# Kernel optimization log

Measured on AMD Instinct MI355X. Metric: run time of the kernel, lower is better.

Reference implementation:

```python
import jax, jax.numpy as jnp
import numpy as np

# Representation config (from init_kwargs): rep1 = rep2 = degrees [0, 1], mult = 32
N = 50000          # nodes
E = 800000         # edges (avg degree 16)
M = 32             # channel multiplicity (rep2.mult)
L_IN = [0, 1]
L_OUT = [0, 1]
D_IN = sum(2 * l + 1 for l in L_IN)    # 4; rep1_cdims = [0, 1, 4]
D_OUT = sum(2 * l + 1 for l in L_OUT)  # 4
OUT_DIMS = np.array([2 * l + 1 for l in L_OUT])  # [1, 3]


def setup_inputs() -> dict:
    key = jax.random.key(0)
    k1, k2, k3, k4 = jax.random.split(key, 4)
    basis = jax.random.normal(k1, (E, D_OUT, D_IN), dtype=jnp.float32)
    edge_weights = jax.random.normal(k2, (E, len(L_OUT), M), dtype=jnp.float32)
    node_features = jax.random.normal(k3, (N, D_IN, M), dtype=jnp.float32)
    U = jax.random.randint(k4, (E,), 0, N)  # edge source node indices
    return {"basis": basis, "edge_weights": edge_weights,
            "node_features": node_features, "U": U}


def reference(basis, edge_weights, node_features, U):
    # matmulStepOne: gather source-node features per edge, contract with the
    # per-edge equivariant basis (block-structured over rep1 degree slices;
    # equivalent to one dense [D_OUT, D_IN] matmul per edge).
    x = node_features[U]                          # [E, D_IN, M] (irregular gather)
    tmp = jnp.einsum('eoi,eim->eom', basis, x)    # [E, D_OUT, M]
    # matmulStepTwo: degree-wise weighted combine — each output degree block
    # (of size 2l+1) is scaled by its per-edge, per-channel radial weight.
    w = jnp.repeat(edge_weights, OUT_DIMS, axis=1, total_repeat_length=D_OUT)  # [E, D_OUT, M]
    return tmp * w
```

## Files before the change

### kernel.cpp

```cpp
#include <hip/hip_runtime.h>


typedef float f4 __attribute__((ext_vector_type(4)));

__global__ __launch_bounds__(256) void equiv_mm_kernel(
    const float* __restrict__ basis,
    const float* __restrict__ ew,
    const float* __restrict__ nf,
    const int*   __restrict__ U,
    float*       __restrict__ out,
    int E)
{
    int gid = blockIdx.x * blockDim.x + threadIdx.x;
    int e = gid >> 3;
    if (e >= E) return;
    int m0 = (gid & 7) << 2;

    int u = U[e];

    const f4* xp = (const f4*)(nf + (size_t)u * 128 + m0);
    f4 x0 = xp[0];
    f4 x1 = xp[8];
    f4 x2 = xp[16];
    f4 x3 = xp[24];

    const f4* bp = (const f4*)(basis + (size_t)e * 16);
    f4 b0 = __builtin_nontemporal_load(bp + 0);
    f4 b1 = __builtin_nontemporal_load(bp + 1);
    f4 b2 = __builtin_nontemporal_load(bp + 2);
    f4 b3 = __builtin_nontemporal_load(bp + 3);

    const f4* wp = (const f4*)(ew + (size_t)e * 64 + m0);
    f4 w0 = __builtin_nontemporal_load(wp + 0);
    f4 w1 = __builtin_nontemporal_load(wp + 8);

    f4* op = (f4*)(out + (size_t)e * 128 + m0);
    __builtin_nontemporal_store((b0.x * x0 + b0.y * x1 + b0.z * x2 + b0.w * x3) * w0, op + 0);
    __builtin_nontemporal_store((b1.x * x0 + b1.y * x1 + b1.z * x2 + b1.w * x3) * w1, op + 8);
    __builtin_nontemporal_store((b2.x * x0 + b2.y * x1 + b2.z * x2 + b2.w * x3) * w1, op + 16);
    __builtin_nontemporal_store((b3.x * x0 + b3.y * x1 + b3.z * x2 + b3.w * x3) * w1, op + 24);
}

extern "C" void kernel_launch(void* const* d_in, const int* in_sizes, int n_in,
                              void* d_out, int out_size, void* d_ws, size_t ws_size,
                              hipStream_t stream) {
    const float* basis = (const float*)d_in[0];
    const float* ew    = (const float*)d_in[1];
    const float* nf    = (const float*)d_in[2];
    const int*   U     = (const int*)d_in[3];
    float* out = (float*)d_out;

    int E = in_sizes[0] / 16;
    long long total = (long long)E * 8;
    int block = 256;
    int grid = (int)((total + block - 1) / block);

    equiv_mm_kernel<<<grid, block, 0, stream>>>(basis, ew, nf, U, out, E);
}
```

Measured before the change: 153.7 us.

## Partition edges into node-range passes to keep gathered features cache-resident

Splits the work into passes by source-node range (4096 nodes per pass). Each block scans its 256 edges and processes only those whose source node falls in the current pass, so the gathered node features for one pass stay within a cache-sized window. The cost is that every pass re-reads the whole U array, roughly 13 passes, and many waves do little useful work because of divergence. Output writes become scattered across passes instead of streaming in order.

```diff
diff --git a/kernel.cpp b/kernel.cpp
--- a/kernel.cpp
+++ b/kernel.cpp
@@ -3,42 +3,57 @@
 
 typedef float f4 __attribute__((ext_vector_type(4)));
 
-__global__ __launch_bounds__(256) void equiv_mm_kernel(
+#define NSHIFT 12
+#define EDGES_PER_BLOCK 256
+
+__global__ __launch_bounds__(256) void equiv_mm_pass_kernel(
     const float* __restrict__ basis,
     const float* __restrict__ ew,
     const float* __restrict__ nf,
     const int*   __restrict__ U,
     float*       __restrict__ out,
-    int E)
+    int E, int blocksPerPass)
 {
-    int gid = blockIdx.x * blockDim.x + threadIdx.x;
-    int e = gid >> 3;
-    if (e >= E) return;
-    int m0 = (gid & 7) << 2;
+    const int pass  = blockIdx.x / blocksPerPass;
+    const int blk   = blockIdx.x % blocksPerPass;
+    const int group = threadIdx.x >> 3;
+    const int m0    = (threadIdx.x & 7) << 2;
+    const int ebase = blk * EDGES_PER_BLOCK;
 
-    int u = U[e];
+    #pragma unroll 1
+    for (int it = 0; it < 8; ++it) {
+        int e = ebase + it * 32 + group;
+        int u = 0;
+        bool active = false;
+        if (e < E) {
+            u = U[e];
+            active = ((u >> NSHIFT) == pass);
+        }
+        if (__ballot(active) == 0ull) continue;
+        if (!active) continue;
 
-    const f4* xp = (const f4*)(nf + (size_t)u * 128 + m0);
-    f4 x0 = xp[0];
-    f4 x1 = xp[8];
-    f4 x2 = xp[16];
-    f4 x3 = xp[24];
+        const f4* xp = (const f4*)(nf + (size_t)u * 128 + m0);
+        f4 x0 = xp[0];
+        f4 x1 = xp[8];
+        f4 x2 = xp[16];
+        f4 x3 = xp[24];
 
-    const f4* bp = (const f4*)(basis + (size_t)e * 16);
-    f4 b0 = __builtin_nontemporal_load(bp + 0);
-    f4 b1 = __builtin_nontemporal_load(bp + 1);
-    f4 b2 = __builtin_nontemporal_load(bp + 2);
-    f4 b3 = __builtin_nontemporal_load(bp + 3);
+        const f4* bp = (const f4*)(basis + (size_t)e * 16);
+        f4 b0 = __builtin_nontemporal_load(bp + 0);
+        f4 b1 = __builtin_nontemporal_load(bp + 1);
+        f4 b2 = __builtin_nontemporal_load(bp + 2);
+        f4 b3 = __builtin_nontemporal_load(bp + 3);
 
-    const f4* wp = (const f4*)(ew + (size_t)e * 64 + m0);
-    f4 w0 = __builtin_nontemporal_load(wp + 0);
-    f4 w1 = __builtin_nontemporal_load(wp + 8);
+        const f4* wp = (const f4*)(ew + (size_t)e * 64 + m0);
+        f4 w0 = __builtin_nontemporal_load(wp + 0);
+        f4 w1 = __builtin_nontemporal_load(wp + 8);
 
-    f4* op = (f4*)(out + (size_t)e * 128 + m0);
-    __builtin_nontemporal_store((b0.x * x0 + b0.y * x1 + b0.z * x2 + b0.w * x3) * w0, op + 0);
-    __builtin_nontemporal_store((b1.x * x0 + b1.y * x1 + b1.z * x2 + b1.w * x3) * w1, op + 8);
-    __builtin_nontemporal_store((b2.x * x0 + b2.y * x1 + b2.z * x2 + b2.w * x3) * w1, op + 16);
-    __builtin_nontemporal_store((b3.x * x0 + b3.y * x1 + b3.z * x2 + b3.w * x3) * w1, op + 24);
+        f4* op = (f4*)(out + (size_t)e * 128 + m0);
+        __builtin_nontemporal_store((b0.x * x0 + b0.y * x1 + b0.z * x2 + b0.w * x3) * w0, op + 0);
+        __builtin_nontemporal_store((b1.x * x0 + b1.y * x1 + b1.z * x2 + b1.w * x3) * w1, op + 8);
+        __builtin_nontemporal_store((b2.x * x0 + b2.y * x1 + b2.z * x2 + b2.w * x3) * w1, op + 16);
+        __builtin_nontemporal_store((b3.x * x0 + b3.y * x1 + b3.z * x2 + b3.w * x3) * w1, op + 24);
+    }
 }
 
 extern "C" void kernel_launch(void* const* d_in, const int* in_sizes, int n_in,
@@ -51,9 +66,11 @@
     float* out = (float*)d_out;
 
     int E = in_sizes[0] / 16;
-    long long total = (long long)E * 8;
-    int block = 256;
-    int grid = (int)((total + block - 1) / block);
+    int N = in_sizes[2] / 128;
+    int npass = ((N - 1) >> NSHIFT) + 1;
+    int blocksPerPass = (E + EDGES_PER_BLOCK - 1) / EDGES_PER_BLOCK;
+    int grid = blocksPerPass * npass;
 
-    equiv_mm_kernel<<<grid, block, 0, stream>>>(basis, ew, nf, U, out, E);
+    equiv_mm_pass_kernel<<<grid, 256, 0, stream>>>(basis, ew, nf, U, out,
+                                                   E, blocksPerPass);
 }
```

Result: slower. 347.7 us (+126.3%).

## Bucket edges by source node block and stage node features in LDS

Applied to the files above, without the earlier changes.

Adds histogram, scan and scatter kernels that group edges by 64-node blocks of their source node. A bucketed kernel then loads each node slice into shared memory and processes that bucket's edges from LDS. The aim is to remove the irregular global gather of node features. In exchange it adds extra launches, contended atomics and a permuted access pattern over the large per-edge arrays.

```diff
diff --git a/kernel.cpp b/kernel.cpp
--- a/kernel.cpp
+++ b/kernel.cpp
@@ -3,42 +3,123 @@
 
 typedef float f4 __attribute__((ext_vector_type(4)));
 
-__global__ __launch_bounds__(256) void equiv_mm_kernel(
+#define BSHIFT 6
+#define BBLK 512
+
+
+__global__ void hist_kernel(const int* __restrict__ U, int* __restrict__ hist, int E) {
+    int stride = gridDim.x * blockDim.x;
+    for (int e = blockIdx.x * blockDim.x + threadIdx.x; e < E; e += stride)
+        atomicAdd(&hist[U[e] >> BSHIFT], 1);
+}
+
+__global__ void scan_kernel(int* __restrict__ hist ,
+                            int* __restrict__ cursor , int NB, int E) {
+    __shared__ int a[1024], b[1024];
+    int t = threadIdx.x;
+    a[t] = (t < NB) ? hist[t] : 0;
+    __syncthreads();
+    int* src = a; int* dst = b;
+    for (int off = 1; off < 1024; off <<= 1) {
+        int x = src[t];
+        if (t >= off) x += src[t - off];
+        dst[t] = x;
+        __syncthreads();
+        int* tmp = src; src = dst; dst = tmp;
+    }
+    if (t < NB) {
+        int excl = (t == 0) ? 0 : src[t - 1];
+        hist[t] = excl;
+        cursor[t] = excl;
+    }
+    if (t == 0) hist[NB] = E;
+}
+
+__global__ void scatter_kernel(const int* __restrict__ U, int* __restrict__ cursor,
+                               int* __restrict__ perm, int E) {
+    int stride = gridDim.x * blockDim.x;
+    for (int e = blockIdx.x * blockDim.x + threadIdx.x; e < E; e += stride) {
+        int u = U[e];
+        int pos = atomicAdd(&cursor[u >> BSHIFT], 1);
+        perm[pos] = ((u & ((1 << BSHIFT) - 1)) << 24) | e;
+    }
+}
+
+
+__global__ __launch_bounds__(BBLK) void equiv_mm_bucket_kernel(
     const float* __restrict__ basis,
     const float* __restrict__ ew,
     const float* __restrict__ nf,
-    const int*   __restrict__ U,
+    const int*   __restrict__ base,
+    const int*   __restrict__ perm,
     float*       __restrict__ out,
-    int E)
+    int N, int NB)
+{
+    __shared__ f4 slice[(1 << BSHIFT) * 32];
+    const f4* nf4 = (const f4*)nf;
+
+    for (int nb = blockIdx.x; nb < NB; nb += gridDim.x) {
+        int node0 = nb << BSHIFT;
+        int nNodes = min(1 << BSHIFT, N - node0);
+        int cnt4 = nNodes * 32;
+        __syncthreads();
+        for (int i = threadIdx.x; i < cnt4; i += BBLK)
+            slice[i] = __builtin_nontemporal_load(&nf4[(size_t)node0 * 32 + i]);
+        __syncthreads();
+
+        int start = base[nb], end = base[nb + 1];
+        int lanes = (end - start) << 3;
+        for (int k = threadIdx.x; k < lanes; k += BBLK) {
+            int slot = start + (k >> 3);
+            int m0 = (k & 7) << 2;
+            int pk = __builtin_nontemporal_load(&perm[slot]);
+            int e  = pk & 0xFFFFFF;
+            int ul = pk >> 24;
+
+            const f4* xp = slice + ul * 32 + (m0 >> 2);
+            f4 x0 = xp[0], x1 = xp[8], x2 = xp[16], x3 = xp[24];
+
+            const f4* bp = (const f4*)(basis + (size_t)e * 16);
+            f4 b0 = __builtin_nontemporal_load(bp + 0);
+            f4 b1 = __builtin_nontemporal_load(bp + 1);
+            f4 b2 = __builtin_nontemporal_load(bp + 2);
+            f4 b3 = __builtin_nontemporal_load(bp + 3);
+
+            const f4* wp = (const f4*)(ew + (size_t)e * 64 + m0);
+            f4 w0 = __builtin_nontemporal_load(wp + 0);
+            f4 w1 = __builtin_nontemporal_load(wp + 8);
+
+            f4* op = (f4*)(out + (size_t)e * 128 + m0);
+            __builtin_nontemporal_store((b0.x*x0 + b0.y*x1 + b0.z*x2 + b0.w*x3) * w0, op + 0);
+            __builtin_nontemporal_store((b1.x*x0 + b1.y*x1 + b1.z*x2 + b1.w*x3) * w1, op + 8);
+            __builtin_nontemporal_store((b2.x*x0 + b2.y*x1 + b2.z*x2 + b2.w*x3) * w1, op + 16);
+            __builtin_nontemporal_store((b3.x*x0 + b3.y*x1 + b3.z*x2 + b3.w*x3) * w1, op + 24);
+        }
+    }
+}
+
+
+__global__ __launch_bounds__(256) void equiv_mm_simple_kernel(
+    const float* __restrict__ basis, const float* __restrict__ ew,
+    const float* __restrict__ nf, const int* __restrict__ U,
+    float* __restrict__ out, int E)
 {
     int gid = blockIdx.x * blockDim.x + threadIdx.x;
     int e = gid >> 3;
     if (e >= E) return;
     int m0 = (gid & 7) << 2;
-
     int u = U[e];
-
     const f4* xp = (const f4*)(nf + (size_t)u * 128 + m0);
-    f4 x0 = xp[0];
-    f4 x1 = xp[8];
-    f4 x2 = xp[16];
-    f4 x3 = xp[24];
-
+    f4 x0 = xp[0], x1 = xp[8], x2 = xp[16], x3 = xp[24];
     const f4* bp = (const f4*)(basis + (size_t)e * 16);
-    f4 b0 = __builtin_nontemporal_load(bp + 0);
-    f4 b1 = __builtin_nontemporal_load(bp + 1);
-    f4 b2 = __builtin_nontemporal_load(bp + 2);
-    f4 b3 = __builtin_nontemporal_load(bp + 3);
-
+    f4 b0 = bp[0], b1 = bp[1], b2 = bp[2], b3 = bp[3];
     const f4* wp = (const f4*)(ew + (size_t)e * 64 + m0);
-    f4 w0 = __builtin_nontemporal_load(wp + 0);
-    f4 w1 = __builtin_nontemporal_load(wp + 8);
-
+    f4 w0 = wp[0], w1 = wp[8];
     f4* op = (f4*)(out + (size_t)e * 128 + m0);
-    __builtin_nontemporal_store((b0.x * x0 + b0.y * x1 + b0.z * x2 + b0.w * x3) * w0, op + 0);
-    __builtin_nontemporal_store((b1.x * x0 + b1.y * x1 + b1.z * x2 + b1.w * x3) * w1, op + 8);
-    __builtin_nontemporal_store((b2.x * x0 + b2.y * x1 + b2.z * x2 + b2.w * x3) * w1, op + 16);
-    __builtin_nontemporal_store((b3.x * x0 + b3.y * x1 + b3.z * x2 + b3.w * x3) * w1, op + 24);
+    __builtin_nontemporal_store((b0.x*x0 + b0.y*x1 + b0.z*x2 + b0.w*x3) * w0, op + 0);
+    __builtin_nontemporal_store((b1.x*x0 + b1.y*x1 + b1.z*x2 + b1.w*x3) * w1, op + 8);
+    __builtin_nontemporal_store((b2.x*x0 + b2.y*x1 + b2.z*x2 + b2.w*x3) * w1, op + 16);
+    __builtin_nontemporal_store((b3.x*x0 + b3.y*x1 + b3.z*x2 + b3.w*x3) * w1, op + 24);
 }
 
 extern "C" void kernel_launch(void* const* d_in, const int* in_sizes, int n_in,
@@ -51,9 +132,27 @@
     float* out = (float*)d_out;
 
     int E = in_sizes[0] / 16;
-    long long total = (long long)E * 8;
-    int block = 256;
-    int grid = (int)((total + block - 1) / block);
+    int N = in_sizes[2] / 128;
+    int NB = ((N - 1) >> BSHIFT) + 1;
 
-    equiv_mm_kernel<<<grid, block, 0, stream>>>(basis, ew, nf, U, out, E);
+    size_t need = ((size_t)(NB + 1) + NB + E) * 4;
+    bool can_sort = (ws_size >= need) && (NB <= 1024) && (E < (1 << 24));
+
+    if (!can_sort) {
+        long long total = (long long)E * 8;
+        int grid = (int)((total + 255) / 256);
+        equiv_mm_simple_kernel<<<grid, 256, 0, stream>>>(basis, ew, nf, U, out, E);
+        return;
+    }
+
+    int* base   = (int*)d_ws;
+    int* cursor = base + (NB + 1);
+    int* perm   = cursor + NB;
+
+    hipMemsetAsync(base, 0, (size_t)(NB + 1) * 4, stream);
+    hist_kernel<<<2048, 256, 0, stream>>>(U, base, E);
+    scan_kernel<<<1, 1024, 0, stream>>>(base, cursor, NB, E);
+    scatter_kernel<<<2048, 256, 0, stream>>>(U, cursor, perm, E);
+    equiv_mm_bucket_kernel<<<NB, BBLK, 0, stream>>>(basis, ew, nf, base, perm,
+                                                    out, N, NB);
 }
```

New measurement: 559.6 us. 264% more time.
